# Optimization experiments

Measured on AMD Instinct MI355X. Metric: run time of the kernel, lower is better.

The kernel has to match this reference:

```python
import jax, jax.numpy as jnp
import numpy as np

NCONF, NATOMS, NCOEFF = 64, 256, 45
NAOV = 12  # 4 p-vectors + 8 d-vectors (3 'diagonal' + 5 'off-diagonal' rows)

# hyperparameters (floats from the forward signature, fixed here)
LOW_S, UP_S = 0.5, 3.5
LOW_R, UP_R = 0.5, 3.5
LOW_A, UP_A = 0.5, 3.5
LOW_Z, UP_Z = 0.19634954, 2.94524311  # ~pi/16 .. 15*pi/16
OETA_S, OETA_R, OETA_A, OZETA = 16.0, 16.0, 8.0, 32.0


def setup_inputs() -> dict:
    key = jax.random.key(0)
    coefficients = jax.random.normal(key, (NCONF, NATOMS, NCOEFF), dtype=jnp.float32)
    return {"coefficients": coefficients, "NOShfS": 16, "NOShfR": 16, "NOShfA": 8, "NOShfZ": 8}


def _orbital_matrix(coefficients):
    n, a, _ = coefficients.shape
    p = coefficients[:, :, 9:21].reshape(n, a, 4, 3)
    d = coefficients[:, :, 21:45].reshape(n, a, 4, 6)
    d = d[..., jnp.array([0, 2, 5, 4, 3, 1])].reshape(n, a, 8, 3)
    # cat([p, d[:, :, :3], d[:, :, 3:]]) == cat([p, d])
    return jnp.concatenate([p, d], axis=2)  # [n, a, 12, 3]


def reference(coefficients, NOShfS, NOShfR, NOShfA, NOShfZ):
    # basis_functions='spd', use_simple_orbital_aev=False, use_angular_info=True
    n, a, _ = coefficients.shape
    om = _orbital_matrix(coefficients)                 # [n, a, 12, 3]
    dist = jnp.linalg.norm(om, axis=-1)                # [n, a, 12]

    shfS = jnp.linspace(LOW_S, UP_S, NOShfS)
    shfR = jnp.linspace(LOW_R, UP_R, NOShfR)
    s_aev = jnp.exp(-OETA_S * (dist[..., None] - shfS) ** 2)   # [n, a, 12, S]
    r_aev = jnp.exp(-OETA_R * (dist[..., None] - shfR) ** 2)   # [n, a, 12, R]
    radial = jnp.concatenate([s_aev, r_aev], axis=-1).reshape(n, a, NAOV * (NOShfS + NOShfR))

    # angles between all AOV pairs (vectorized version of the nested i<j loop)
    zero_mask = jnp.all(jnp.abs(om) < 1e-12, axis=-1)          # [n, a, 12]
    safe_d = jnp.where(zero_mask, 1.0, dist)
    nv = jnp.where(zero_mask[..., None], 0.0, om / safe_d[..., None])  # normalized AOVs
    iu, ju = np.triu_indices(NAOV, k=1)                        # 66 pairs, i-major order
    cos_ang = jnp.einsum('napk,napk->nap', nv[:, :, iu], nv[:, :, ju])  # [n, a, 66]
    angles = jnp.arccos(0.95 * cos_ang)
    avdist = 0.5 * (dist[:, :, iu] + dist[:, :, ju])           # [n, a, 66]

    shfZ = jnp.linspace(LOW_Z, UP_Z, NOShfZ)
    shfA = jnp.linspace(LOW_A, UP_A, NOShfA)
    factor1 = ((1.0 + jnp.cos(angles[..., None] - shfZ)) * 0.5) ** OZETA      # [n, a, 66, Z]
    factor2 = jnp.exp(-OETA_A * (avdist[..., None] - shfA) ** 2)              # [n, a, 66, A]
    angular = 2.0 * factor1[..., :, None] * factor2[..., None, :]             # [n, a, 66, Z, A]
    angular = angular.reshape(n, a, angles.shape[2] * NOShfZ * NOShfA)

    return jnp.concatenate([radial, angular], axis=-1)  # [n, a, 12*(S+R) + 66*Z*A]
```

## Files before the change

### kernel.cpp

```cpp
#include <hip/hip_runtime.h>
#include <math.h>

#define NCONF  64
#define NATOMS 256
#define NCOEFF 45
#define NAOV   12
#define NPAIR  66
#define NZ     8
#define NA     8
#define RAD    384
#define ANG    4224
#define TOT    4608

__constant__ unsigned char c_iu[NPAIR] = {
    0,0,0,0,0,0,0,0,0,0,0,
    1,1,1,1,1,1,1,1,1,1,
    2,2,2,2,2,2,2,2,2,
    3,3,3,3,3,3,3,3,
    4,4,4,4,4,4,4,
    5,5,5,5,5,5,
    6,6,6,6,6,
    7,7,7,7,
    8,8,8,
    9,9,
    10
};
__constant__ unsigned char c_ju[NPAIR] = {
    1,2,3,4,5,6,7,8,9,10,11,
    2,3,4,5,6,7,8,9,10,11,
    3,4,5,6,7,8,9,10,11,
    4,5,6,7,8,9,10,11,
    5,6,7,8,9,10,11,
    6,7,8,9,10,11,
    7,8,9,10,11,
    8,9,10,11,
    9,10,11,
    10,11,
    11
};

__constant__ float c_shfS[16] = {
    0.5f, 0.7f, 0.9f, 1.1f, 1.3f, 1.5f, 1.7f, 1.9f,
    2.1f, 2.3f, 2.5f, 2.7f, 2.9f, 3.1f, 3.3f, 3.5f
};
__constant__ float c_shfA[8] = {
    0.5f, 0.92857142857f, 1.35714285714f, 1.78571428571f,
    2.21428571429f, 2.64285714286f, 3.07142857143f, 3.5f
};
__constant__ float c_cosZ[8] = {
     0.98078528f,  0.83146961f,  0.55557023f,  0.19509032f,
    -0.19509032f, -0.55557023f, -0.83146961f, -0.98078528f
};
__constant__ float c_sinZ[8] = {
    0.19509032f, 0.55557023f, 0.83146961f, 0.98078528f,
    0.98078528f, 0.83146961f, 0.55557023f, 0.19509032f
};


__global__ __launch_bounds__(256)
void OrbitalAEVComputer_40492951667225_kernel(const float* __restrict__ coef,
                                              float* __restrict__ out) {
    const int atom = blockIdx.x;
    const float* c = coef + (size_t)atom * NCOEFF;
    float* o = out + (size_t)atom * TOT;
    const int t = threadIdx.x;

    __shared__ float s_dist[NAOV];
    __shared__ float s_nv[NAOV][3];
    __shared__ float s_c95[NPAIR];
    __shared__ float s_sin[NPAIR];
    __shared__ float s_avd[NPAIR];
    __shared__ float s_f1[NPAIR * NZ];
    __shared__ float s_f2[NPAIR * NA];

    if (t < NAOV) {
        float x, y, z;
        if (t < 4) {
            x = c[9 + 3 * t]; y = c[10 + 3 * t]; z = c[11 + 3 * t];
        } else {
            int r = (t - 4) >> 1, h = (t - 4) & 1;
            const int base = 21 + 6 * r;
            if (h == 0) { x = c[base + 0]; y = c[base + 2]; z = c[base + 5]; }
            else        { x = c[base + 4]; y = c[base + 3]; z = c[base + 1]; }
        }
        float d = sqrtf(x * x + y * y + z * z);
        bool zm = (fabsf(x) < 1e-12f) && (fabsf(y) < 1e-12f) && (fabsf(z) < 1e-12f);
        float inv = zm ? 0.0f : 1.0f / d;
        s_dist[t] = d;
        s_nv[t][0] = x * inv;
        s_nv[t][1] = y * inv;
        s_nv[t][2] = z * inv;
    }
    __syncthreads();

    if (t < NPAIR) {
        int i = c_iu[t], j = c_ju[t];
        float cang = s_nv[i][0] * s_nv[j][0]
                   + s_nv[i][1] * s_nv[j][1]
                   + s_nv[i][2] * s_nv[j][2];
        float c95 = 0.95f * cang;
        s_c95[t] = c95;
        s_sin[t] = sqrtf(fmaxf(1.0f - c95 * c95, 0.0f));
        s_avd[t] = 0.5f * (s_dist[i] + s_dist[j]);
    }
    __syncthreads();

    for (int idx = t; idx < NPAIR * NZ; idx += 256) {
        int q = idx >> 3, k = idx & 7;
        float cosa = fmaf(s_c95[q], c_cosZ[k], s_sin[q] * c_sinZ[k]);
        float x = 0.5f * (1.0f + cosa);
        x = x * x; x = x * x; x = x * x; x = x * x; x = x * x;
        s_f1[idx] = x;
        float dd = s_avd[q] - c_shfA[k];
        s_f2[idx] = __expf(-8.0f * dd * dd);
    }
    __syncthreads();

    if (t < 96) {
        int e = t * 4;
        int p = e >> 5;
        float d = s_dist[p];
        int k0 = e & 31;
        float4 v;
        {
            float df = d - c_shfS[(k0 + 0) & 15]; v.x = __expf(-16.0f * df * df);
        }
        {
            float df = d - c_shfS[(k0 + 1) & 15]; v.y = __expf(-16.0f * df * df);
        }
        {
            float df = d - c_shfS[(k0 + 2) & 15]; v.z = __expf(-16.0f * df * df);
        }
        {
            float df = d - c_shfS[(k0 + 3) & 15]; v.w = __expf(-16.0f * df * df);
        }
        reinterpret_cast<float4*>(o)[t] = v;
    }

    for (int idx4 = t; idx4 < ANG / 4; idx4 += 256) {
        int e = idx4 * 4;
        int q = e >> 6;
        int z = (e >> 3) & 7;
        int a0 = e & 7;
        float f1 = 2.0f * s_f1[q * 8 + z];
        const float* f2 = &s_f2[q * 8 + a0];
        float4 v;
        v.x = f1 * f2[0];
        v.y = f1 * f2[1];
        v.z = f1 * f2[2];
        v.w = f1 * f2[3];
        reinterpret_cast<float4*>(o + RAD)[idx4] = v;
    }
}

extern "C" void kernel_launch(void* const* d_in, const int* in_sizes, int n_in,
                              void* d_out, int out_size, void* d_ws, size_t ws_size,
                              hipStream_t stream) {
    const float* coef = (const float*)d_in[0];
    float* out = (float*)d_out;
    OrbitalAEVComputer_40492951667225_kernel<<<dim3(NCONF * NATOMS), dim3(256), 0, stream>>>(coef, out);
}
```

Before: 311.0 us.

## Process eight atoms per block with double-buffered shared stages and merged phases

Each block now handles eight atoms in a loop with double-buffered shared memory, which cuts the block count eightfold. The pair-setup stage is merged into the f1/f2 computation, leaving two barriers per atom instead of three. Radial terms are precomputed into shared memory and written in one unified float4 store loop with the angular block. The aim is to amortize block launch and setup overhead for this store-bound kernel, at the cost of fewer blocks and serial per-atom barriers within each block.

```diff
diff --git a/kernel.cpp b/kernel.cpp
--- a/kernel.cpp
+++ b/kernel.cpp
@@ -6,11 +6,10 @@
 #define NCOEFF 45
 #define NAOV   12
 #define NPAIR  66
-#define NZ     8
-#define NA     8
 #define RAD    384
 #define ANG    4224
 #define TOT    4608
+#define APB    8
 
 __constant__ unsigned char c_iu[NPAIR] = {
     0,0,0,0,0,0,0,0,0,0,0,
@@ -56,100 +55,96 @@
     0.98078528f, 0.83146961f, 0.55557023f, 0.19509032f
 };
 
-
-__global__ __launch_bounds__(256)
+__global__ __launch_bounds__(256, 8)
 void OrbitalAEVComputer_40492951667225_kernel(const float* __restrict__ coef,
                                               float* __restrict__ out) {
-    const int atom = blockIdx.x;
-    const float* c = coef + (size_t)atom * NCOEFF;
-    float* o = out + (size_t)atom * TOT;
     const int t = threadIdx.x;
 
-    __shared__ float s_dist[NAOV];
-    __shared__ float s_nv[NAOV][3];
-    __shared__ float s_c95[NPAIR];
-    __shared__ float s_sin[NPAIR];
-    __shared__ float s_avd[NPAIR];
-    __shared__ float s_f1[NPAIR * NZ];
-    __shared__ float s_f2[NPAIR * NA];
+    __shared__ float s_dist[2][NAOV];
+    __shared__ float s_nv[2][NAOV][3];
+    __shared__ float s_rad[2][NAOV * 16];
+    __shared__ float s_f1[2][NPAIR * 8];
+    __shared__ float s_f2[2][NPAIR * 8];
 
-    if (t < NAOV) {
-        float x, y, z;
-        if (t < 4) {
-            x = c[9 + 3 * t]; y = c[10 + 3 * t]; z = c[11 + 3 * t];
-        } else {
-            int r = (t - 4) >> 1, h = (t - 4) & 1;
-            const int base = 21 + 6 * r;
-            if (h == 0) { x = c[base + 0]; y = c[base + 2]; z = c[base + 5]; }
-            else        { x = c[base + 4]; y = c[base + 3]; z = c[base + 1]; }
+    const int atom0 = blockIdx.x * APB;
+
+    for (int a = 0; a < APB; ++a) {
+        const int buf = a & 1;
+        const int atom = atom0 + a;
+        const float* c = coef + (size_t)atom * NCOEFF;
+
+        if (t < NAOV) {
+            float x, y, z;
+            if (t < 4) {
+                x = c[9 + 3 * t]; y = c[10 + 3 * t]; z = c[11 + 3 * t];
+            } else {
+                int r = (t - 4) >> 1, h = (t - 4) & 1;
+                const float* b = c + 21 + 6 * r;
+                if (h == 0) { x = b[0]; y = b[2]; z = b[5]; }
+                else        { x = b[4]; y = b[3]; z = b[1]; }
+            }
+            float d = sqrtf(x * x + y * y + z * z);
+            bool zm = (fabsf(x) < 1e-12f) && (fabsf(y) < 1e-12f) && (fabsf(z) < 1e-12f);
+            float inv = zm ? 0.0f : 1.0f / d;
+            s_dist[buf][t] = d;
+            s_nv[buf][t][0] = x * inv;
+            s_nv[buf][t][1] = y * inv;
+            s_nv[buf][t][2] = z * inv;
         }
-        float d = sqrtf(x * x + y * y + z * z);
-        bool zm = (fabsf(x) < 1e-12f) && (fabsf(y) < 1e-12f) && (fabsf(z) < 1e-12f);
-        float inv = zm ? 0.0f : 1.0f / d;
-        s_dist[t] = d;
-        s_nv[t][0] = x * inv;
-        s_nv[t][1] = y * inv;
-        s_nv[t][2] = z * inv;
-    }
-    __syncthreads();
+        __syncthreads();
 
-    if (t < NPAIR) {
-        int i = c_iu[t], j = c_ju[t];
-        float cang = s_nv[i][0] * s_nv[j][0]
-                   + s_nv[i][1] * s_nv[j][1]
-                   + s_nv[i][2] * s_nv[j][2];
-        float c95 = 0.95f * cang;
-        s_c95[t] = c95;
-        s_sin[t] = sqrtf(fmaxf(1.0f - c95 * c95, 0.0f));
-        s_avd[t] = 0.5f * (s_dist[i] + s_dist[j]);
-    }
-    __syncthreads();
+        for (int idx = t; idx < 1248; idx += 256) {
+            if (idx < 192) {
+                int p = idx >> 4, k = idx & 15;
+                float dd = s_dist[buf][p] - c_shfS[k];
+                s_rad[buf][idx] = __expf(-16.0f * dd * dd);
+            } else if (idx < 720) {
+                int jj = idx - 192;
+                int q = jj >> 3, k = jj & 7;
+                int i1 = c_iu[q], j1 = c_ju[q];
+                float cang = s_nv[buf][i1][0] * s_nv[buf][j1][0]
+                           + s_nv[buf][i1][1] * s_nv[buf][j1][1]
+                           + s_nv[buf][i1][2] * s_nv[buf][j1][2];
+                float c95 = 0.95f * cang;
+                float sn  = sqrtf(fmaxf(1.0f - c95 * c95, 0.0f));
+                float cosa = fmaf(c95, c_cosZ[k], sn * c_sinZ[k]);
+                float x = 0.5f * (1.0f + cosa);
+                x = x * x; x = x * x; x = x * x; x = x * x; x = x * x;
+                s_f1[buf][jj] = x;
+            } else {
+                int jj = idx - 720;
+                int q = jj >> 3, k = jj & 7;
+                int i1 = c_iu[q], j1 = c_ju[q];
+                float avd = 0.5f * (s_dist[buf][i1] + s_dist[buf][j1]);
+                float dd = avd - c_shfA[k];
+                s_f2[buf][jj] = __expf(-8.0f * dd * dd);
+            }
+        }
+        __syncthreads();
 
-    for (int idx = t; idx < NPAIR * NZ; idx += 256) {
-        int q = idx >> 3, k = idx & 7;
-        float cosa = fmaf(s_c95[q], c_cosZ[k], s_sin[q] * c_sinZ[k]);
-        float x = 0.5f * (1.0f + cosa);
-        x = x * x; x = x * x; x = x * x; x = x * x; x = x * x;
-        s_f1[idx] = x;
-        float dd = s_avd[q] - c_shfA[k];
-        s_f2[idx] = __expf(-8.0f * dd * dd);
-    }
-    __syncthreads();
-
-    if (t < 96) {
-        int e = t * 4;
-        int p = e >> 5;
-        float d = s_dist[p];
-        int k0 = e & 31;
-        float4 v;
-        {
-            float df = d - c_shfS[(k0 + 0) & 15]; v.x = __expf(-16.0f * df * df);
+        float* o = out + (size_t)atom * TOT;
+        for (int idx4 = t; idx4 < TOT / 4; idx4 += 256) {
+            float4 v;
+            if (idx4 < 96) {
+                int e = idx4 * 4;
+                int p = e >> 5;
+                int k0 = e & 31;
+                const float* src = &s_rad[buf][p * 16 + (k0 & 15)];
+                v = *reinterpret_cast<const float4*>(src);
+            } else {
+                int e = (idx4 - 96) * 4;
+                int q = e >> 6;
+                int z = (e >> 3) & 7;
+                int a0 = e & 7;
+                float f1v = 2.0f * s_f1[buf][q * 8 + z];
+                const float4 f2v = *reinterpret_cast<const float4*>(&s_f2[buf][q * 8 + a0]);
+                v.x = f1v * f2v.x;
+                v.y = f1v * f2v.y;
+                v.z = f1v * f2v.z;
+                v.w = f1v * f2v.w;
+            }
+            reinterpret_cast<float4*>(o)[idx4] = v;
         }
-        {
-            float df = d - c_shfS[(k0 + 1) & 15]; v.y = __expf(-16.0f * df * df);
-        }
-        {
-            float df = d - c_shfS[(k0 + 2) & 15]; v.z = __expf(-16.0f * df * df);
-        }
-        {
-            float df = d - c_shfS[(k0 + 3) & 15]; v.w = __expf(-16.0f * df * df);
-        }
-        reinterpret_cast<float4*>(o)[t] = v;
-    }
-
-    for (int idx4 = t; idx4 < ANG / 4; idx4 += 256) {
-        int e = idx4 * 4;
-        int q = e >> 6;
-        int z = (e >> 3) & 7;
-        int a0 = e & 7;
-        float f1 = 2.0f * s_f1[q * 8 + z];
-        const float* f2 = &s_f2[q * 8 + a0];
-        float4 v;
-        v.x = f1 * f2[0];
-        v.y = f1 * f2[1];
-        v.z = f1 * f2[2];
-        v.w = f1 * f2[3];
-        reinterpret_cast<float4*>(o + RAD)[idx4] = v;
     }
 }
 
@@ -158,5 +153,5 @@
                               hipStream_t stream) {
     const float* coef = (const float*)d_in[0];
     float* out = (float*)d_out;
-    OrbitalAEVComputer_40492951667225_kernel<<<dim3(NCONF * NATOMS), dim3(256), 0, stream>>>(coef, out);
+    OrbitalAEVComputer_40492951667225_kernel<<<dim3(NCONF * NATOMS / APB), dim3(256), 0, stream>>>(coef, out);
 }
```

Result: slower. 320.6 us (+3.1%).
